# Performance work log

Hardware: AMD Instinct MI355X
Metric: run time of the kernel (lower is better)

The kernel has to match this reference:

```python
import jax, jax.numpy as jnp
import numpy as np

N_NODES = 50000
LN_EPS = 1e-5


def gcn_conv(x, src, dst, norm, W, b):
    # PyG GCNConv: h = x @ W, then symmetric-normalized scatter-add, then bias.
    h = x @ W                                   # [N, out]
    msg = h[src] * norm[:, None]                # [E+N, out] gathered, scaled
    out = jax.ops.segment_sum(msg, dst, num_segments=N_NODES)
    return out + b


def layer_norm(x, gamma, beta):
    mu = jnp.mean(x, axis=-1, keepdims=True)
    var = jnp.var(x, axis=-1, keepdims=True)
    return (x - mu) * jax.lax.rsqrt(var + LN_EPS) * gamma + beta


def setup_inputs() -> dict:
    key = jax.random.key(0)
    ks = jax.random.split(key, 8)
    N, E, D = N_NODES, 1600000, 128
    x = jax.random.normal(ks[0], (N, D), dtype=jnp.float32)
    edge_index = jax.random.randint(ks[1], (2, E), 0, N, dtype=jnp.int64)
    s = 1.0 / np.sqrt(D)
    return {
        "x": x,
        "edge_index": edge_index,
        "W1": jax.random.uniform(ks[2], (D, D), jnp.float32, -s, s),
        "b1": jnp.zeros((D,), jnp.float32),
        "g1": jnp.ones((D,), jnp.float32),
        "be1": jnp.zeros((D,), jnp.float32),
        "W2": jax.random.uniform(ks[3], (D, D), jnp.float32, -s, s),
        "b2": jnp.zeros((D,), jnp.float32),
        "g2": jnp.ones((D,), jnp.float32),
        "be2": jnp.zeros((D,), jnp.float32),
    }


def reference(x, edge_index, W1, b1, g1, be1, W2, b2, g2, be2):
    # Add self-loops (PyG GCNConv default add_self_loops=True)
    sl = jnp.arange(N_NODES, dtype=edge_index.dtype)
    src = jnp.concatenate([edge_index[0], sl])
    dst = jnp.concatenate([edge_index[1], sl])
    # Symmetric normalization: deg^{-1/2}[src] * deg^{-1/2}[dst]
    deg = jax.ops.segment_sum(jnp.ones_like(src, dtype=x.dtype), dst,
                              num_segments=N_NODES)
    dinv = jnp.where(deg > 0, jax.lax.rsqrt(deg), 0.0)
    norm = dinv[src] * dinv[dst]

    h = gcn_conv(x, src, dst, norm, W1, b1)
    h = jax.nn.elu(layer_norm(h, g1, be1))
    h = gcn_conv(h, src, dst, norm, W2, b2)
    h = jax.nn.elu(layer_norm(h, g2, be2))
    return h
```

## Files before the change

### kernel.cpp

```cpp
#include <hip/hip_runtime.h>
#include <hip/hip_bf16.h>
#include <math.h>

#define N_NODES 50000
#define D 128
#define LN_EPS 1e-5f
#define NB 391
#define CHUNK 4096
#define TB 32
#define HB 512
#define PB 391
#define GB2 391

typedef unsigned int u32;
typedef unsigned short u16;
typedef __attribute__((ext_vector_type(8))) short bf16x8;
typedef __attribute__((ext_vector_type(8))) unsigned short u16x8;
typedef __attribute__((ext_vector_type(4))) float f32x4;

static __device__ __forceinline__ u16 f2bf(float f) {
    union { float f; unsigned u; } v; v.f = f;
    unsigned r = v.u + 0x7fff + ((v.u >> 16) & 1);
    return (u16)(r >> 16);
}
static __device__ __forceinline__ float bf2f(u16 b) {
    union { unsigned u; float f; } v; v.u = ((unsigned)b) << 16;
    return v.f;
}
static __device__ __forceinline__ bf16x8 packf8(const float* p) {
    float4 f0 = *(const float4*)p;
    float4 f1 = *(const float4*)(p + 4);
    bf16x8 r;
    r[0] = (short)f2bf(f0.x); r[1] = (short)f2bf(f0.y);
    r[2] = (short)f2bf(f0.z); r[3] = (short)f2bf(f0.w);
    r[4] = (short)f2bf(f1.x); r[5] = (short)f2bf(f1.y);
    r[6] = (short)f2bf(f1.z); r[7] = (short)f2bf(f1.w);
    return r;
}

static __device__ __forceinline__ void agg_core8(
        const u16* __restrict__ H, const u16* __restrict__ csr_src,
        const float* __restrict__ dinv, int s, int cnt, int c0, float dn,
        float* __restrict__ a) {
    float b[8];
#pragma unroll
    for (int i = 0; i < 8; ++i) { a[i] = 0.f; b[i] = 0.f; }
    const u16* cp = csr_src + s;
    int j = 0;
    for (; j + 8 <= cnt; j += 8) {
        u32 i0 = cp[j],     i1 = cp[j + 1], i2 = cp[j + 2], i3 = cp[j + 3];
        u32 i4 = cp[j + 4], i5 = cp[j + 5], i6 = cp[j + 6], i7 = cp[j + 7];
        u16x8 g0 = *(const u16x8*)&H[(size_t)i0 * D + c0];
        u16x8 g1 = *(const u16x8*)&H[(size_t)i1 * D + c0];
        u16x8 g2 = *(const u16x8*)&H[(size_t)i2 * D + c0];
        u16x8 g3 = *(const u16x8*)&H[(size_t)i3 * D + c0];
        u16x8 g4 = *(const u16x8*)&H[(size_t)i4 * D + c0];
        u16x8 g5 = *(const u16x8*)&H[(size_t)i5 * D + c0];
        u16x8 g6 = *(const u16x8*)&H[(size_t)i6 * D + c0];
        u16x8 g7 = *(const u16x8*)&H[(size_t)i7 * D + c0];
        float w0 = dinv[i0] * dn, w1 = dinv[i1] * dn;
        float w2 = dinv[i2] * dn, w3 = dinv[i3] * dn;
        float w4 = dinv[i4] * dn, w5 = dinv[i5] * dn;
        float w6 = dinv[i6] * dn, w7 = dinv[i7] * dn;
#pragma unroll
        for (int i = 0; i < 8; ++i) {
            a[i] = fmaf(w0, bf2f(g0[i]), a[i]);
            b[i] = fmaf(w1, bf2f(g1[i]), b[i]);
            a[i] = fmaf(w2, bf2f(g2[i]), a[i]);
            b[i] = fmaf(w3, bf2f(g3[i]), b[i]);
            a[i] = fmaf(w4, bf2f(g4[i]), a[i]);
            b[i] = fmaf(w5, bf2f(g5[i]), b[i]);
            a[i] = fmaf(w6, bf2f(g6[i]), a[i]);
            b[i] = fmaf(w7, bf2f(g7[i]), b[i]);
        }
    }
    for (; j < cnt; ++j) {
        u32 i0 = cp[j];
        u16x8 g0 = *(const u16x8*)&H[(size_t)i0 * D + c0];
        float w0 = dinv[i0] * dn;
#pragma unroll
        for (int i = 0; i < 8; ++i) a[i] = fmaf(w0, bf2f(g0[i]), a[i]);
    }
#pragma unroll
    for (int i = 0; i < 8; ++i) a[i] += b[i];
}

static __device__ __forceinline__ void ln_elu8(
        float* __restrict__ a, int c0,
        const float* __restrict__ bias, const float* __restrict__ gamma,
        const float* __restrict__ beta) {
    float4 bv0 = *(const float4*)&bias[c0];
    float4 bv1 = *(const float4*)&bias[c0 + 4];
    a[0] += bv0.x; a[1] += bv0.y; a[2] += bv0.z; a[3] += bv0.w;
    a[4] += bv1.x; a[5] += bv1.y; a[6] += bv1.z; a[7] += bv1.w;
    float sum = 0.f, sq = 0.f;
#pragma unroll
    for (int i = 0; i < 8; ++i) { sum += a[i]; sq = fmaf(a[i], a[i], sq); }
#pragma unroll
    for (int m = 8; m > 0; m >>= 1) {
        sum += __shfl_xor(sum, m, 64);
        sq  += __shfl_xor(sq,  m, 64);
    }
    float mean = sum * (1.f / 128.f);
    float var  = sq * (1.f / 128.f) - mean * mean;
    float rstd = rsqrtf(var + LN_EPS);
    float4 gv0 = *(const float4*)&gamma[c0];
    float4 gv1 = *(const float4*)&gamma[c0 + 4];
    float4 ev0 = *(const float4*)&beta[c0];
    float4 ev1 = *(const float4*)&beta[c0 + 4];
    float gg[8] = {gv0.x, gv0.y, gv0.z, gv0.w, gv1.x, gv1.y, gv1.z, gv1.w};
    float ee[8] = {ev0.x, ev0.y, ev0.z, ev0.w, ev1.x, ev1.y, ev1.z, ev1.w};
#pragma unroll
    for (int i = 0; i < 8; ++i) {
        float y = (a[i] - mean) * rstd * gg[i] + ee[i];
        a[i] = y > 0.f ? y : expm1f(y);
    }
}

__global__ __launch_bounds__(256) void trans_hist(const float* __restrict__ W1,
                                                  const float* __restrict__ W2,
                                                  u16* __restrict__ W1T,
                                                  u16* __restrict__ W2T,
                                                  const int* __restrict__ dstA,
                                                  u32* __restrict__ bucketCount, int E) {
    __shared__ u32 hist[NB];

    if (blockIdx.x < TB) {
        __shared__ u16 tile[32][33];
        int mat  = blockIdx.x >> 4;
        int tl   = blockIdx.x & 15;
        int bi   = (tl >> 2) * 32;
        int bj   = (tl & 3) * 32;
        const float* w = mat ? W2 : W1;
        u16* wt = mat ? W2T : W1T;
        int t = threadIdx.x;
        int lr = t >> 5, lc = t & 31;
#pragma unroll
        for (int pass = 0; pass < 4; ++pass) {
            int r = lr + pass * 8;
            tile[r][lc] = f2bf(w[(size_t)(bi + r) * D + bj + lc]);
        }
        __syncthreads();
#pragma unroll
        for (int pass = 0; pass < 4; ++pass) {
            int c = lr + pass * 8;
            wt[(size_t)(bj + c) * D + bi + lc] = tile[lc][c];
        }
        return;
    }
    for (int b = threadIdx.x; b < NB; b += 256) hist[b] = 0;
    __syncthreads();
    int stride = HB * 256;
    for (int e = (blockIdx.x - TB) * 256 + threadIdx.x; e < E; e += stride)
        atomicAdd(&hist[((u32)dstA[e]) >> 7], 1u);
    __syncthreads();
    for (int b = threadIdx.x; b < NB; b += 256)
        if (hist[b]) atomicAdd(&bucketCount[b], hist[b]);
}

__global__ __launch_bounds__(512) void part_gemm(const int* __restrict__ srcA,
                                                 const int* __restrict__ dstA,
                                                 const u32* __restrict__ bucketCount,
                                                 u32* __restrict__ relCursor,
                                                 u32* __restrict__ ebuf, int E,
                                                 const float* __restrict__ X,
                                                 const u16* __restrict__ W1T,
                                                 u16* __restrict__ H) {
    __shared__ u32 sc[512];
    __shared__ u32 ebS[NB], cntA[NB], cntB[NB], base[NB];
    int t = threadIdx.x;

    if (blockIdx.x >= PB) {
        int lane = t & 63;
        int wid  = t >> 6;
        int r    = lane & 15;
        int kg   = lane >> 4;
        int rb   = (blockIdx.x - PB) * 8 + wid;
        if (rb >= N_NODES / 16) return;
        int row0 = rb * 16;
        const float* xp = X + (size_t)(row0 + r) * D + kg * 8;
        bf16x8 a0 = packf8(xp);      bf16x8 a1 = packf8(xp + 32);
        bf16x8 a2 = packf8(xp + 64); bf16x8 a3 = packf8(xp + 96);
#pragma unroll
        for (int tile = 0; tile < 8; ++tile) {
            const u16* wp = W1T + (size_t)(tile * 16 + r) * D + kg * 8;
            f32x4 acc = {0.f, 0.f, 0.f, 0.f};
            acc = __builtin_amdgcn_mfma_f32_16x16x32_bf16(a0, *(const bf16x8*)(wp),      acc, 0, 0, 0);
            acc = __builtin_amdgcn_mfma_f32_16x16x32_bf16(a1, *(const bf16x8*)(wp + 32), acc, 0, 0, 0);
            acc = __builtin_amdgcn_mfma_f32_16x16x32_bf16(a2, *(const bf16x8*)(wp + 64), acc, 0, 0, 0);
            acc = __builtin_amdgcn_mfma_f32_16x16x32_bf16(a3, *(const bf16x8*)(wp + 96), acc, 0, 0, 0);
#pragma unroll
            for (int i = 0; i < 4; ++i)
                H[(size_t)(row0 + kg * 4 + i) * D + tile * 16 + r] = f2bf(acc[i]);
        }
        return;
    }

    u32 bc = (t < NB) ? bucketCount[t] : 0u;
    sc[t] = bc;
    for (int b = t; b < NB; b += 512) { cntA[b] = 0; cntB[b] = 0; }
    __syncthreads();
    for (int off = 1; off < 512; off <<= 1) {
        u32 v = sc[t] + ((t >= off) ? sc[t - off] : 0u);
        __syncthreads();
        sc[t] = v;
        __syncthreads();
    }
    if (t < NB) ebS[t] = sc[t] - bc;
    __syncthreads();

    int e0 = blockIdx.x * CHUNK;
    int e1 = min(e0 + CHUNK, E);
    for (int e = e0 + t; e < e1; e += 512)
        atomicAdd(&cntA[((u32)dstA[e]) >> 7], 1u);
    __syncthreads();
    for (int b = t; b < NB; b += 512)
        if (cntA[b]) base[b] = ebS[b] + atomicAdd(&relCursor[b], cntA[b]);
    __syncthreads();
    for (int e = e0 + t; e < e1; e += 512) {
        u32 d = (u32)dstA[e], sv = (u32)srcA[e];
        u32 b = d >> 7;
        u32 off = atomicAdd(&cntB[b], 1u);
        ebuf[base[b] + off] = (sv << 16) | d;
    }
}

__global__ __launch_bounds__(256) void bucket_build(const u32* __restrict__ ebuf,
                                                    const u32* __restrict__ bucketCount,
                                                    u16* __restrict__ csr_src,
                                                    int* __restrict__ startArr,
                                                    float* __restrict__ dinv) {
    int b = blockIdx.x, t = threadIdx.x;
    __shared__ u32 red[256];
    __shared__ u32 cnt[128], sc[128], cur[128];
    u32 partial = 0;
    for (int i = t; i < b; i += 256) partial += bucketCount[i];
    red[t] = partial;
    if (t < 128) cnt[t] = 0;
    __syncthreads();
    for (int off = 128; off > 0; off >>= 1) {
        if (t < off) red[t] += red[t + off];
        __syncthreads();
    }
    u32 eb0 = red[0];
    u32 eb1 = eb0 + bucketCount[b];
    u32 cs  = eb0 + 128u * (u32)b;

    int nodeBase = b << 7;
    int nNodes = min(128, N_NODES - nodeBase);
    for (u32 e = eb0 + t; e < eb1; e += 256)
        atomicAdd(&cnt[ebuf[e] & 127u], 1u);
    __syncthreads();
    u32 myCnt = 0;
    if (t < 128) {
        myCnt = (t < nNodes) ? cnt[t] + 1u : 0u;
        sc[t] = myCnt;
    }
    __syncthreads();
    for (int off = 1; off < 128; off <<= 1) {
        u32 v = 0;
        if (t < 128) v = sc[t] + ((t >= off) ? sc[t - off] : 0u);
        __syncthreads();
        if (t < 128) sc[t] = v;
        __syncthreads();
    }
    if (t < nNodes) {
        u32 excl = sc[t] - myCnt;
        int i = nodeBase + t;
        startArr[i] = (int)(cs + excl);
        dinv[i] = rsqrtf((float)myCnt);
        csr_src[cs + excl] = (u16)i;
        cur[t] = excl + 1u;
        if (b == NB - 1 && t == nNodes - 1)
            startArr[N_NODES] = (int)(cs + sc[t]);
    }
    __syncthreads();
    for (u32 e = eb0 + t; e < eb1; e += 256) {
        u32 p = ebuf[e];
        u32 pos = atomicAdd(&cur[p & 127u], 1u);
        csr_src[cs + pos] = (u16)(p >> 16);
    }
}

__global__ __launch_bounds__(256) void agg_gemm(
        const u16* __restrict__ H, const u16* __restrict__ csr_src,
        const int* __restrict__ startArr, const float* __restrict__ dinv,
        const float* __restrict__ bias, const float* __restrict__ gamma,
        const float* __restrict__ beta,
        const u16* __restrict__ W2T, u16* __restrict__ H2) {
    __shared__ __align__(16) u16 X2[16][136];

    int t = threadIdx.x;
    int grp = t >> 4;
    int l   = t & 15;
    int c0  = l * 8;
    int node = blockIdx.x * 16 + grp;
    int s   = startArr[node];
    int cnt = startArr[node + 1] - s;
    float dn = dinv[node];

    float a[8];
    agg_core8(H, csr_src, dinv, s, cnt, c0, dn, a);
    ln_elu8(a, c0, bias, gamma, beta);

    u16x8 o;
#pragma unroll
    for (int i = 0; i < 8; ++i) o[i] = f2bf(a[i]);
    *(u16x8*)&X2[grp][c0] = o;
    __syncthreads();

    int lane = t & 63;
    int wv   = t >> 6;
    int r    = lane & 15;
    int kg   = lane >> 4;
    int row0 = blockIdx.x * 16;

    const u16* xp = &X2[r][kg * 8];
    bf16x8 a0f = *(const bf16x8*)(xp);
    bf16x8 a1f = *(const bf16x8*)(xp + 32);
    bf16x8 a2f = *(const bf16x8*)(xp + 64);
    bf16x8 a3f = *(const bf16x8*)(xp + 96);
#pragma unroll
    for (int tile = wv; tile < 8; tile += 4) {
        const u16* wp = W2T + (size_t)(tile * 16 + r) * D + kg * 8;
        f32x4 acc = {0.f, 0.f, 0.f, 0.f};
        acc = __builtin_amdgcn_mfma_f32_16x16x32_bf16(a0f, *(const bf16x8*)(wp),      acc, 0, 0, 0);
        acc = __builtin_amdgcn_mfma_f32_16x16x32_bf16(a1f, *(const bf16x8*)(wp + 32), acc, 0, 0, 0);
        acc = __builtin_amdgcn_mfma_f32_16x16x32_bf16(a2f, *(const bf16x8*)(wp + 64), acc, 0, 0, 0);
        acc = __builtin_amdgcn_mfma_f32_16x16x32_bf16(a3f, *(const bf16x8*)(wp + 96), acc, 0, 0, 0);
#pragma unroll
        for (int i = 0; i < 4; ++i)
            H2[(size_t)(row0 + kg * 4 + i) * D + tile * 16 + r] = f2bf(acc[i]);
    }
}

__global__ __launch_bounds__(256) void agg_ln_elu(
        const u16* __restrict__ H, const u16* __restrict__ csr_src,
        const int* __restrict__ startArr, const float* __restrict__ dinv,
        const float* __restrict__ bias, const float* __restrict__ gamma,
        const float* __restrict__ beta, float* __restrict__ out) {
    int t = threadIdx.x;
    int node = blockIdx.x * 16 + (t >> 4);
    int l    = t & 15;
    int c0   = l * 8;
    int s    = startArr[node];
    int cnt  = startArr[node + 1] - s;
    float dn = dinv[node];

    float a[8];
    agg_core8(H, csr_src, dinv, s, cnt, c0, dn, a);
    ln_elu8(a, c0, bias, gamma, beta);

    f32x4 o0 = {a[0], a[1], a[2], a[3]};
    f32x4 o1 = {a[4], a[5], a[6], a[7]};
    float* op = out + (size_t)node * D + c0;
    __builtin_nontemporal_store(o0, (f32x4*)op);
    __builtin_nontemporal_store(o1, (f32x4*)(op + 4));
}

extern "C" void kernel_launch(void* const* d_in, const int* in_sizes, int n_in,
                              void* d_out, int out_size, void* d_ws, size_t ws_size,
                              hipStream_t stream) {
    const float* x   = (const float*)d_in[0];
    const int*  eidx = (const int*)d_in[1];
    const float* W1  = (const float*)d_in[2];
    const float* b1  = (const float*)d_in[3];
    const float* g1  = (const float*)d_in[4];
    const float* be1 = (const float*)d_in[5];
    const float* W2  = (const float*)d_in[6];
    const float* b2  = (const float*)d_in[7];
    const float* g2  = (const float*)d_in[8];
    const float* be2 = (const float*)d_in[9];

    int E = in_sizes[1] / 2;
    const int* srcA = eidx;
    const int* dstA = eidx + E;

    char* p = (char*)d_ws;
    auto alloc = [&](size_t bytes) {
        char* r = p;
        p += (bytes + 255) & ~(size_t)255;
        return r;
    };
    u32*   ctr      = (u32*)alloc((size_t)1024 * 4);
    u32*   ebuf     = (u32*)alloc((size_t)E * 4);
    u16*   csr_src  = (u16*)alloc((size_t)(E + N_NODES) * 2);
    int*   startArr = (int*)alloc((size_t)(N_NODES + 1) * 4);
    float* dinv     = (float*)alloc((size_t)N_NODES * 4);
    u16*   w1t      = (u16*)alloc((size_t)D * D * 2);
    u16*   w2t      = (u16*)alloc((size_t)D * D * 2);
    u16*   h        = (u16*)alloc((size_t)N_NODES * D * 2);
    u16*   h2       = (u16*)alloc((size_t)N_NODES * D * 2);
    float* outp     = (float*)d_out;

    u32* bucketCount = ctr;
    u32* relCursor   = ctr + 512;

    int fb = N_NODES / 16;

    hipError_t e0 = hipMemsetAsync(ctr, 0, 1024 * 4, stream);
    (void)e0;
    trans_hist  <<<TB + HB, 256, 0, stream>>>(W1, W2, w1t, w2t, dstA, bucketCount, E);
    part_gemm   <<<PB + GB2, 512, 0, stream>>>(srcA, dstA, bucketCount, relCursor,
                                               ebuf, E, x, w1t, h);
    bucket_build<<<NB, 256, 0, stream>>>(ebuf, bucketCount, csr_src, startArr, dinv);
    agg_gemm    <<<fb, 256, 0, stream>>>(h, csr_src, startArr, dinv,
                                         b1, g1, be1, w2t, h2);
    agg_ln_elu  <<<fb, 256, 0, stream>>>(h2, csr_src, startArr, dinv,
                                         b2, g2, be2, outp);
}
```

Measured before the change: 278.9 us.

## Precompute per-edge norm weights and pad CSR rows to multiples of eight

```diff
diff --git a/kernel.cpp b/kernel.cpp
--- a/kernel.cpp
+++ b/kernel.cpp
@@ -38,48 +38,82 @@
     return r;
 }
 
-static __device__ __forceinline__ void agg_core8(
+static __device__ __forceinline__ void agg_core16(
         const u16* __restrict__ H, const u16* __restrict__ csr_src,
-        const float* __restrict__ dinv, int s, int cnt, int c0, float dn,
+        const float* __restrict__ csr_w, int s, int cnt, int c0,
         float* __restrict__ a) {
     float b[8];
 #pragma unroll
     for (int i = 0; i < 8; ++i) { a[i] = 0.f; b[i] = 0.f; }
     const u16* cp = csr_src + s;
+    const float* wp = csr_w + s;
     int j = 0;
-    for (; j + 8 <= cnt; j += 8) {
-        u32 i0 = cp[j],     i1 = cp[j + 1], i2 = cp[j + 2], i3 = cp[j + 3];
-        u32 i4 = cp[j + 4], i5 = cp[j + 5], i6 = cp[j + 6], i7 = cp[j + 7];
-        u16x8 g0 = *(const u16x8*)&H[(size_t)i0 * D + c0];
-        u16x8 g1 = *(const u16x8*)&H[(size_t)i1 * D + c0];
-        u16x8 g2 = *(const u16x8*)&H[(size_t)i2 * D + c0];
-        u16x8 g3 = *(const u16x8*)&H[(size_t)i3 * D + c0];
-        u16x8 g4 = *(const u16x8*)&H[(size_t)i4 * D + c0];
-        u16x8 g5 = *(const u16x8*)&H[(size_t)i5 * D + c0];
-        u16x8 g6 = *(const u16x8*)&H[(size_t)i6 * D + c0];
-        u16x8 g7 = *(const u16x8*)&H[(size_t)i7 * D + c0];
-        float w0 = dinv[i0] * dn, w1 = dinv[i1] * dn;
-        float w2 = dinv[i2] * dn, w3 = dinv[i3] * dn;
-        float w4 = dinv[i4] * dn, w5 = dinv[i5] * dn;
-        float w6 = dinv[i6] * dn, w7 = dinv[i7] * dn;
+    for (; j + 16 <= cnt; j += 16) {
+        u16x8 I0 = *(const u16x8*)(cp + j);
+        u16x8 I1 = *(const u16x8*)(cp + j + 8);
+        f32x4 W0 = *(const f32x4*)(wp + j);
+        f32x4 W1 = *(const f32x4*)(wp + j + 4);
+        f32x4 W2 = *(const f32x4*)(wp + j + 8);
+        f32x4 W3 = *(const f32x4*)(wp + j + 12);
+        u16x8 g0 = *(const u16x8*)&H[(size_t)(u32)I0[0] * D + c0];
+        u16x8 g1 = *(const u16x8*)&H[(size_t)(u32)I0[1] * D + c0];
+        u16x8 g2 = *(const u16x8*)&H[(size_t)(u32)I0[2] * D + c0];
+        u16x8 g3 = *(const u16x8*)&H[(size_t)(u32)I0[3] * D + c0];
+        u16x8 g4 = *(const u16x8*)&H[(size_t)(u32)I0[4] * D + c0];
+        u16x8 g5 = *(const u16x8*)&H[(size_t)(u32)I0[5] * D + c0];
+        u16x8 g6 = *(const u16x8*)&H[(size_t)(u32)I0[6] * D + c0];
+        u16x8 g7 = *(const u16x8*)&H[(size_t)(u32)I0[7] * D + c0];
+        u16x8 g8  = *(const u16x8*)&H[(size_t)(u32)I1[0] * D + c0];
+        u16x8 g9  = *(const u16x8*)&H[(size_t)(u32)I1[1] * D + c0];
+        u16x8 g10 = *(const u16x8*)&H[(size_t)(u32)I1[2] * D + c0];
+        u16x8 g11 = *(const u16x8*)&H[(size_t)(u32)I1[3] * D + c0];
+        u16x8 g12 = *(const u16x8*)&H[(size_t)(u32)I1[4] * D + c0];
+        u16x8 g13 = *(const u16x8*)&H[(size_t)(u32)I1[5] * D + c0];
+        u16x8 g14 = *(const u16x8*)&H[(size_t)(u32)I1[6] * D + c0];
+        u16x8 g15 = *(const u16x8*)&H[(size_t)(u32)I1[7] * D + c0];
 #pragma unroll
         for (int i = 0; i < 8; ++i) {
-            a[i] = fmaf(w0, bf2f(g0[i]), a[i]);
-            b[i] = fmaf(w1, bf2f(g1[i]), b[i]);
-            a[i] = fmaf(w2, bf2f(g2[i]), a[i]);
-            b[i] = fmaf(w3, bf2f(g3[i]), b[i]);
-            a[i] = fmaf(w4, bf2f(g4[i]), a[i]);
-            b[i] = fmaf(w5, bf2f(g5[i]), b[i]);
-            a[i] = fmaf(w6, bf2f(g6[i]), a[i]);
-            b[i] = fmaf(w7, bf2f(g7[i]), b[i]);
-        }
-    }
-    for (; j < cnt; ++j) {
-        u32 i0 = cp[j];
-        u16x8 g0 = *(const u16x8*)&H[(size_t)i0 * D + c0];
-        float w0 = dinv[i0] * dn;
-#pragma unroll
-        for (int i = 0; i < 8; ++i) a[i] = fmaf(w0, bf2f(g0[i]), a[i]);
+            a[i] = fmaf(W0.x, bf2f(g0[i]),  a[i]);
+            b[i] = fmaf(W0.y, bf2f(g1[i]),  b[i]);
+            a[i] = fmaf(W0.z, bf2f(g2[i]),  a[i]);
+            b[i] = fmaf(W0.w, bf2f(g3[i]),  b[i]);
+            a[i] = fmaf(W1.x, bf2f(g4[i]),  a[i]);
+            b[i] = fmaf(W1.y, bf2f(g5[i]),  b[i]);
+            a[i] = fmaf(W1.z, bf2f(g6[i]),  a[i]);
+            b[i] = fmaf(W1.w, bf2f(g7[i]),  b[i]);
+            a[i] = fmaf(W2.x, bf2f(g8[i]),  a[i]);
+            b[i] = fmaf(W2.y, bf2f(g9[i]),  b[i]);
+            a[i] = fmaf(W2.z, bf2f(g10[i]), a[i]);
+            b[i] = fmaf(W2.w, bf2f(g11[i]), b[i]);
+            a[i] = fmaf(W3.x, bf2f(g12[i]), a[i]);
+            b[i] = fmaf(W3.y, bf2f(g13[i]), b[i]);
+            a[i] = fmaf(W3.z, bf2f(g14[i]), a[i]);
+            b[i] = fmaf(W3.w, bf2f(g15[i]), b[i]);
+        }
+    }
+    if (j < cnt) {
+        u16x8 I0 = *(const u16x8*)(cp + j);
+        f32x4 W0 = *(const f32x4*)(wp + j);
+        f32x4 W1 = *(const f32x4*)(wp + j + 4);
+        u16x8 g0 = *(const u16x8*)&H[(size_t)(u32)I0[0] * D + c0];
+        u16x8 g1 = *(const u16x8*)&H[(size_t)(u32)I0[1] * D + c0];
+        u16x8 g2 = *(const u16x8*)&H[(size_t)(u32)I0[2] * D + c0];
+        u16x8 g3 = *(const u16x8*)&H[(size_t)(u32)I0[3] * D + c0];
+        u16x8 g4 = *(const u16x8*)&H[(size_t)(u32)I0[4] * D + c0];
+        u16x8 g5 = *(const u16x8*)&H[(size_t)(u32)I0[5] * D + c0];
+        u16x8 g6 = *(const u16x8*)&H[(size_t)(u32)I0[6] * D + c0];
+        u16x8 g7 = *(const u16x8*)&H[(size_t)(u32)I0[7] * D + c0];
+#pragma unroll
+        for (int i = 0; i < 8; ++i) {
+            a[i] = fmaf(W0.x, bf2f(g0[i]), a[i]);
+            b[i] = fmaf(W0.y, bf2f(g1[i]), b[i]);
+            a[i] = fmaf(W0.z, bf2f(g2[i]), a[i]);
+            b[i] = fmaf(W0.w, bf2f(g3[i]), b[i]);
+            a[i] = fmaf(W1.x, bf2f(g4[i]), a[i]);
+            b[i] = fmaf(W1.y, bf2f(g5[i]), b[i]);
+            a[i] = fmaf(W1.z, bf2f(g6[i]), a[i]);
+            b[i] = fmaf(W1.w, bf2f(g7[i]), b[i]);
+        }
     }
 #pragma unroll
     for (int i = 0; i < 8; ++i) a[i] += b[i];
@@ -225,14 +259,14 @@
     }
 }
 
-__global__ __launch_bounds__(256) void bucket_build(const u32* __restrict__ ebuf,
-                                                    const u32* __restrict__ bucketCount,
-                                                    u16* __restrict__ csr_src,
-                                                    int* __restrict__ startArr,
-                                                    float* __restrict__ dinv) {
+__global__ __launch_bounds__(256) void bb_deg(const u32* __restrict__ ebuf,
+                                              const u32* __restrict__ bucketCount,
+                                              int* __restrict__ startArr,
+                                              u16* __restrict__ cntArr,
+                                              float* __restrict__ dinv) {
     int b = blockIdx.x, t = threadIdx.x;
     __shared__ u32 red[256];
-    __shared__ u32 cnt[128], sc[128], cur[128];
+    __shared__ u32 cnt[128], sc[128];
     u32 partial = 0;
     for (int i = t; i < b; i += 256) partial += bucketCount[i];
     red[t] = partial;
@@ -244,17 +278,17 @@
     }
     u32 eb0 = red[0];
     u32 eb1 = eb0 + bucketCount[b];
-    u32 cs  = eb0 + 128u * (u32)b;
+    u32 cs  = (eb0 + 1032u * (u32)b + 7u) & ~7u;
 
     int nodeBase = b << 7;
     int nNodes = min(128, N_NODES - nodeBase);
     for (u32 e = eb0 + t; e < eb1; e += 256)
         atomicAdd(&cnt[ebuf[e] & 127u], 1u);
     __syncthreads();
-    u32 myCnt = 0;
+    u32 pc = 0;
     if (t < 128) {
-        myCnt = (t < nNodes) ? cnt[t] + 1u : 0u;
-        sc[t] = myCnt;
+        pc = (t < nNodes) ? ((cnt[t] + 1u + 7u) & ~7u) : 0u;
+        sc[t] = pc;
     }
     __syncthreads();
     for (int off = 1; off < 128; off <<= 1) {
@@ -265,26 +299,70 @@
         __syncthreads();
     }
     if (t < nNodes) {
-        u32 excl = sc[t] - myCnt;
         int i = nodeBase + t;
-        startArr[i] = (int)(cs + excl);
-        dinv[i] = rsqrtf((float)myCnt);
-        csr_src[cs + excl] = (u16)i;
-        cur[t] = excl + 1u;
-        if (b == NB - 1 && t == nNodes - 1)
-            startArr[N_NODES] = (int)(cs + sc[t]);
+        startArr[i] = (int)(cs + sc[t] - pc);
+        cntArr[i] = (u16)pc;
+        dinv[i] = rsqrtf((float)(cnt[t] + 1u));
+    }
+}
+
+__global__ __launch_bounds__(256) void bb_fill(const u32* __restrict__ ebuf,
+                                               const u32* __restrict__ bucketCount,
+                                               const int* __restrict__ startArr,
+                                               const float* __restrict__ dinv,
+                                               u16* __restrict__ csr_src,
+                                               float* __restrict__ csr_w) {
+    int b = blockIdx.x, t = threadIdx.x;
+    __shared__ u32 red[256];
+    __shared__ u32 cur[128];
+    __shared__ float dloc[128];
+    u32 partial = 0;
+    for (int i = t; i < b; i += 256) partial += bucketCount[i];
+    red[t] = partial;
+    __syncthreads();
+    for (int off = 128; off > 0; off >>= 1) {
+        if (t < off) red[t] += red[t + off];
+        __syncthreads();
+    }
+    u32 eb0 = red[0];
+    u32 eb1 = eb0 + bucketCount[b];
+
+    int nodeBase = b << 7;
+    int nNodes = min(128, N_NODES - nodeBase);
+    if (t < nNodes) {
+        int i = nodeBase + t;
+        u32 sa = (u32)startArr[i];
+        float di = dinv[i];
+        dloc[t] = di;
+        csr_src[sa] = (u16)i;
+        csr_w[sa] = di * di;
+        cur[t] = sa + 1u;
     }
     __syncthreads();
     for (u32 e = eb0 + t; e < eb1; e += 256) {
         u32 p = ebuf[e];
-        u32 pos = atomicAdd(&cur[p & 127u], 1u);
-        csr_src[cs + pos] = (u16)(p >> 16);
+        u32 node = p & 127u;
+        u32 src  = p >> 16;
+        u32 pos = atomicAdd(&cur[node], 1u);
+        csr_src[pos] = (u16)src;
+        csr_w[pos] = dinv[src] * dloc[node];
+    }
+    __syncthreads();
+    if (t < nNodes) {
+        u32 sa = (u32)startArr[nodeBase + t];
+        u32 used = cur[t] - sa;
+        u32 end = sa + ((used + 7u) & ~7u);
+        for (u32 pos = cur[t]; pos < end; ++pos) {
+            csr_src[pos] = 0;
+            csr_w[pos] = 0.f;
+        }
     }
 }
 
 __global__ __launch_bounds__(256) void agg_gemm(
         const u16* __restrict__ H, const u16* __restrict__ csr_src,
-        const int* __restrict__ startArr, const float* __restrict__ dinv,
+        const float* __restrict__ csr_w, const int* __restrict__ startArr,
+        const u16* __restrict__ cntArr,
         const float* __restrict__ bias, const float* __restrict__ gamma,
         const float* __restrict__ beta,
         const u16* __restrict__ W2T, u16* __restrict__ H2) {
@@ -296,11 +374,10 @@
     int c0  = l * 8;
     int node = blockIdx.x * 16 + grp;
     int s   = startArr[node];
-    int cnt = startArr[node + 1] - s;
-    float dn = dinv[node];
+    int cnt = cntArr[node];
 
     float a[8];
-    agg_core8(H, csr_src, dinv, s, cnt, c0, dn, a);
+    agg_core16(H, csr_src, csr_w, s, cnt, c0, a);
     ln_elu8(a, c0, bias, gamma, beta);
 
     u16x8 o;
@@ -336,7 +413,8 @@
 
 __global__ __launch_bounds__(256) void agg_ln_elu(
         const u16* __restrict__ H, const u16* __restrict__ csr_src,
-        const int* __restrict__ startArr, const float* __restrict__ dinv,
+        const float* __restrict__ csr_w, const int* __restrict__ startArr,
+        const u16* __restrict__ cntArr,
         const float* __restrict__ bias, const float* __restrict__ gamma,
         const float* __restrict__ beta, float* __restrict__ out) {
     int t = threadIdx.x;
@@ -344,11 +422,10 @@
     int l    = t & 15;
     int c0   = l * 8;
     int s    = startArr[node];
-    int cnt  = startArr[node + 1] - s;
-    float dn = dinv[node];
+    int cnt  = cntArr[node];
 
     float a[8];
-    agg_core8(H, csr_src, dinv, s, cnt, c0, dn, a);
+    agg_core16(H, csr_src, csr_w, s, cnt, c0, a);
     ln_elu8(a, c0, bias, gamma, beta);
 
     f32x4 o0 = {a[0], a[1], a[2], a[3]};
@@ -376,6 +453,8 @@
     const int* srcA = eidx;
     const int* dstA = eidx + E;
 
+    size_t csrCap = (size_t)E + 1032u * NB + 64;
+
     char* p = (char*)d_ws;
     auto alloc = [&](size_t bytes) {
         char* r = p;
@@ -384,8 +463,10 @@
     };
     u32*   ctr      = (u32*)alloc((size_t)1024 * 4);
     u32*   ebuf     = (u32*)alloc((size_t)E * 4);
-    u16*   csr_src  = (u16*)alloc((size_t)(E + N_NODES) * 2);
-    int*   startArr = (int*)alloc((size_t)(N_NODES + 1) * 4);
+    u16*   csr_src  = (u16*)alloc(csrCap * 2);
+    float* csr_w    = (float*)alloc(csrCap * 4);
+    int*   startArr = (int*)alloc((size_t)N_NODES * 4);
+    u16*   cntArr   = (u16*)alloc((size_t)N_NODES * 2);
     float* dinv     = (float*)alloc((size_t)N_NODES * 4);
     u16*   w1t      = (u16*)alloc((size_t)D * D * 2);
     u16*   w2t      = (u16*)alloc((size_t)D * D * 2);
@@ -403,9 +484,11 @@
     trans_hist  <<<TB + HB, 256, 0, stream>>>(W1, W2, w1t, w2t, dstA, bucketCount, E);
     part_gemm   <<<PB + GB2, 512, 0, stream>>>(srcA, dstA, bucketCount, relCursor,
                                                ebuf, E, x, w1t, h);
-    bucket_build<<<NB, 256, 0, stream>>>(ebuf, bucketCount, csr_src, startArr, dinv);
-    agg_gemm    <<<fb, 256, 0, stream>>>(h, csr_src, startArr, dinv,
+    bb_deg      <<<NB, 256, 0, stream>>>(ebuf, bucketCount, startArr, cntArr, dinv);
+    bb_fill     <<<NB, 256, 0, stream>>>(ebuf, bucketCount, startArr, dinv,
+                                         csr_src, csr_w);
+    agg_gemm    <<<fb, 256, 0, stream>>>(h, csr_src, csr_w, startArr, cntArr,
                                          b1, g1, be1, w2t, h2);
-    agg_ln_elu  <<<fb, 256, 0, stream>>>(h2, csr_src, startArr, dinv,
+    agg_ln_elu  <<<fb, 256, 0, stream>>>(h2, csr_src, csr_w, startArr, cntArr,
                                          b2, g2, be2, outp);
 }
```

Result: slower. 293.8 us (+5.4%).
